# Optimization experiments

Measured on AMD Instinct MI355X. Metric: run time of the kernel, lower is better.

Reference implementation:

```python
import jax, jax.numpy as jnp
import numpy as np

B, SQ, SE, SI, SEI = 16, 512, 512, 256, 768
D, H = 1024, 16
DK = D // H
L1, L2 = 0.5, 0.5
NEG = -1e30  # stand-in for -inf masked_fill


def setup_inputs() -> dict:
    key = jax.random.key(0)
    ks = jax.random.split(key, 32)
    f = lambda i, shp: jax.random.normal(ks[i], shp, dtype=jnp.float32)
    w = lambda i: f(i, (D, D)) * (1.0 / np.sqrt(D))
    b = lambda i: jnp.zeros((D,), jnp.float32)
    inp = {
        'q': f(0, (B, SQ, D)),
        'k_e': f(1, (B, SE, D)), 'v_e': f(2, (B, SE, D)),
        'k_i': f(3, (B, SI, D)), 'v_i': f(4, (B, SI, D)),
        'k_ei': f(5, (B, SEI, D)), 'v_ei': f(6, (B, SEI, D)),
        'mask_e': jax.random.randint(ks[7], (B, SQ, SE), 0, 2) == 1,
        'mask_ei': jax.random.randint(ks[8], (B, SQ, SEI), 0, 2) == 1,
        'e_padding_mask': jax.random.randint(ks[9], (B, SE), 0, 2) == 1,
        'ei_padding_mask': jax.random.randint(ks[10], (B, SEI), 0, 2) == 1,
        'Wq': w(11), 'bq': b(11),
        'Wke': w(12), 'bke': b(12), 'Wve': w(13), 'bve': b(13),
        'Wki': w(14), 'bki': b(14), 'Wvi': w(15), 'bvi': b(15),
        'Wkei': w(16), 'bkei': b(16), 'Wvei': w(17), 'bvei': b(17),
        'Wout': w(18), 'bout': b(18),
    }
    return inp


def _proj(x, W, b):
    # (B, S, D) -> (B, H, S, DK)
    B_, S_, _ = x.shape
    return (x @ W + b).reshape(B_, S_, H, DK).transpose(0, 2, 1, 3)


def _attn(qh, kh, vh, mask, pad_mask):
    # qh: (B,H,Sq,DK), kh/vh: (B,H,Sk,DK)
    s = jnp.einsum('bhqd,bhkd->bhqk', qh, kh) / np.sqrt(DK)
    if mask is not None:
        s = jnp.where(mask[:, None, :, :], NEG, s)
    if pad_mask is not None:
        s = jnp.where(pad_mask[:, None, None, :], NEG, s)
    w = jax.nn.softmax(s, axis=-1)
    # dropout in original is applied to a discarded temp (eval / no-op)
    return jnp.einsum('bhqk,bhkd->bhqd', w, vh), w


def reference(q, k_e, k_i, k_ei, v_e, v_i, v_ei,
              mask_e, mask_ei, e_padding_mask, ei_padding_mask,
              Wq, bq, Wke, bke, Wve, bve, Wki, bki, Wvi, bvi,
              Wkei, bkei, Wvei, bvei, Wout, bout):
    qh = _proj(q, Wq, bq)
    o_e, aw_e = _attn(qh, _proj(k_e, Wke, bke), _proj(v_e, Wve, bve), mask_e, e_padding_mask)
    o_i, aw_i = _attn(qh, _proj(k_i, Wki, bki), _proj(v_i, Wvi, bvi), None, None)
    o_ei, _ = _attn(qh, _proj(k_ei, Wkei, bkei), _proj(v_ei, Wvei, bvei), mask_ei, ei_padding_mask)
    scores = o_e + L1 * o_i + L2 * o_ei  # (B,H,Sq,DK)
    concat = scores.transpose(0, 2, 1, 3).reshape(B, SQ, D)
    output = concat @ Wout + bout
    return output, aw_e, aw_i
```

## Files before the change

kernel.cpp:

```cpp
#include <hip/hip_runtime.h>
#include <stdint.h>

typedef __attribute__((ext_vector_type(8))) short bf16x8;
typedef __attribute__((ext_vector_type(4))) short s16x4;
typedef __attribute__((ext_vector_type(4))) float f32x4;

__device__ __forceinline__ short f2bf(float f){
  unsigned x = __float_as_uint(f);
  unsigned r = (x + 0x7fffu + ((x >> 16) & 1u)) >> 16;
  return (short)r;
}

__device__ __forceinline__ void g2l16(const void* g, void* l){
  __builtin_amdgcn_global_load_lds(
      (const __attribute__((address_space(1))) unsigned int*)(unsigned long long)(uintptr_t)g,
      (__attribute__((address_space(3))) unsigned int*)(unsigned int)(uintptr_t)l,
      16, 0, 0);
}

struct C3 { const float* in[3]; short* out[3]; };
__global__ __launch_bounds__(256) void cvt3(C3 c){
  const float* __restrict__ in = c.in[blockIdx.z];
  short* __restrict__ out = c.out[blockIdx.z];
  const int i = blockIdx.x * 256 + threadIdx.x;
  const float4* p = (const float4*)in + (size_t)i * 2;
  const float4 a = p[0], b = p[1];
  bf16x8 v;
  v[0] = f2bf(a.x); v[1] = f2bf(a.y); v[2] = f2bf(a.z); v[3] = f2bf(a.w);
  v[4] = f2bf(b.x); v[5] = f2bf(b.y); v[6] = f2bf(b.z); v[7] = f2bf(b.w);
  *(bf16x8*)(out + (size_t)i * 8) = v;
}

__global__ __launch_bounds__(256)
void make_bits(const int* __restrict__ mask, const int* __restrict__ pad,
               unsigned* __restrict__ bits, int SK){
  const int s = blockIdx.x * 256 + threadIdx.x;
  const size_t row = blockIdx.y;
  const int b = (int)(row >> 9);
  const bool v = (mask[row * SK + s] != 0) || (pad[(size_t)b * SK + s] != 0);
  unsigned long long bal = __ballot(v);
  const int lane = threadIdx.x & 63;
  if ((lane & 31) == 0)
    bits[(row * SK + s) >> 5] = (unsigned)(bal >> (lane & 32));
}

struct W8 { const float* w[8]; };
__global__ __launch_bounds__(256) void pack_w8(W8 ws8, short* __restrict__ out){
  const int m = blockIdx.y;
  const float* __restrict__ W = ws8.w[m];
  short* o = out + (size_t)m * 1048576 + (size_t)blockIdx.x * 4096;
  const int kt = blockIdx.x & 31, nt = blockIdx.x >> 5;
  const int t = threadIdx.x;
  #pragma unroll
  for (int i = 0; i < 16; ++i){
    int flat = i * 256 + t;
    int kl = flat >> 7;
    int nl = flat & 127;
    o[nl * 32 + kl] = f2bf(W[(size_t)(kt * 32 + kl) * 1024 + nt * 128 + nl]);
  }
}

struct GSeg { const short* A; const short* Wp; const float* bias; void* C; int om; int S; };
struct G3 { GSeg s[3]; };
__global__ __launch_bounds__(256)
void gemm128b(G3 g){
  const GSeg sg = g.s[blockIdx.z];
  __shared__ short sA[2][4096];
  __shared__ short sB[2][4096];
  const int t = threadIdx.x;
  const int m0 = blockIdx.x * 128;
  const int nt = blockIdx.y;
  const int n0 = nt * 128;
  const int w = t >> 6, lane = t & 63, lr = lane & 15, lg = lane >> 4;
  const int wm = (w >> 1) * 64, wn = (w & 1) * 64;

  const int arow  = t >> 2;
  const int acol8 = (t & 3) * 8;
  const short* Ag = sg.A + (size_t)(m0 + arow) * 1024 + acol8;
  const short* Bg = sg.Wp + (size_t)nt * 32 * 4096 + t * 8;

  f32x4 acc[4][4] = {};

  {
    g2l16(Ag, sA[0] + t * 8);
    g2l16(Ag + 64 * 1024, sA[0] + 2048 + t * 8);
    g2l16(Bg, sB[0] + t * 8);
    g2l16(Bg + 2048, sB[0] + 2048 + t * 8);
  }

  int cur = 0;
  for (int kt = 0; kt < 32; ++kt){
    __syncthreads();
    if (kt < 31){
      const int kn = kt + 1;
      g2l16(Ag + kn * 32, sA[cur ^ 1] + t * 8);
      g2l16(Ag + 64 * 1024 + kn * 32, sA[cur ^ 1] + 2048 + t * 8);
      const short* bt = Bg + (size_t)kn * 4096;
      g2l16(bt, sB[cur ^ 1] + t * 8);
      g2l16(bt + 2048, sB[cur ^ 1] + 2048 + t * 8);
    }

    bf16x8 af[4], bfr[4];
    #pragma unroll
    for (int mi = 0; mi < 4; ++mi)
      af[mi] = *(const bf16x8*)&sA[cur][(wm + mi * 16 + lr) * 32 + lg * 8];
    #pragma unroll
    for (int ni = 0; ni < 4; ++ni)
      bfr[ni] = *(const bf16x8*)&sB[cur][(wn + ni * 16 + lr) * 32 + lg * 8];
    #pragma unroll
    for (int mi = 0; mi < 4; ++mi)
      #pragma unroll
      for (int ni = 0; ni < 4; ++ni)
        acc[mi][ni] = __builtin_amdgcn_mfma_f32_16x16x32_bf16(
            af[mi], bfr[ni], acc[mi][ni], 0, 0, 0);
    cur ^= 1;
  }

  #pragma unroll
  for (int ni = 0; ni < 4; ++ni){
    const int n = n0 + wn + ni * 16 + lr;
    const float bv = sg.bias[n];
    #pragma unroll
    for (int mi = 0; mi < 4; ++mi){
      const int mb = m0 + wm + mi * 16 + lg * 4;
      if (sg.om == 0){
        short* C = (short*)sg.C;
        #pragma unroll
        for (int j = 0; j < 4; ++j)
          C[(size_t)(mb + j) * 1024 + n] = f2bf(acc[mi][ni][j] + bv);
      } else if (sg.om == 1){
        short* C = (short*)sg.C;
        const int bb = mb / sg.S, sb = mb % sg.S;
        const int hh = n >> 6, dk = n & 63;
        s16x4 pk;
        #pragma unroll
        for (int j = 0; j < 4; ++j) pk[j] = f2bf(acc[mi][ni][j] + bv);
        *(s16x4*)&((short*)sg.C)[(((size_t)bb * 16 + hh) * 64 + dk) * sg.S + sb] = pk;
      } else {
        float* C = (float*)sg.C;
        #pragma unroll
        for (int j = 0; j < 4; ++j)
          C[(size_t)(mb + j) * 1024 + n] = acc[mi][ni][j] + bv;
      }
    }
  }
}

template<int SK, bool HAS_BIAS, bool SINGLE>
__device__ __forceinline__ void attn_mod(
    const short* __restrict__ Kp, const short* __restrict__ Vt,
    const unsigned* __restrict__ bits, float* __restrict__ aw,
    const bf16x8 (&qf)[2], f32x4 (&tot)[4], float wgt,
    short* sK, short* sV, short* sPw,
    int b, int h, int qw, int w, int lane, int lr, int lg){
  constexpr int NT  = SK / 128;
  constexpr int SKW = SK / 32;

  const int kchunk = (lane & 7) ^ ((lane >> 3) & 7);
  const short* Ksrc = Kp + ((size_t)b * SK + w * 32 + (lane >> 3)) * 1024 + h * 64 + kchunk * 8;
  short* sKd = sK + w * 2048 + lane * 8;
  short* sVd = sV + w * 2048 + lane * 8;
  const short* Vsrc = Vt + ((size_t)(b * 16 + h)) * 64 * SK;

  const unsigned* bitrow[4];
  if (HAS_BIAS){
    #pragma unroll
    for (int j = 0; j < 4; ++j)
      bitrow[j] = bits + ((size_t)(b * 512 + qw + lg * 4 + j)) * SKW;
  }

  float lrow[4];
  #pragma unroll
  for (int j = 0; j < 4; ++j) lrow[j] = 0.f;
  f32x4 acco[4] = {};

  if (!SINGLE){
    for (int tt = 0; tt < NT; ++tt){
      const int s0 = tt * 128;
      __syncthreads();
      #pragma unroll
      for (int i = 0; i < 4; ++i)
        g2l16(Ksrc + ((size_t)s0 + i * 8) * 1024, sKd + i * 512);
      __syncthreads();

      f32x4 accs[8];
      #pragma unroll
      for (int si = 0; si < 8; ++si){
        f32x4 a = {};
        #pragma unroll
        for (int dt = 0; dt < 2; ++dt){
          bf16x8 kf = *(const bf16x8*)&sK[(si * 16 + lr) * 64 + ((dt * 4 + lg) ^ (lr & 7)) * 8];
          a = __builtin_amdgcn_mfma_f32_16x16x32_bf16(qf[dt], kf, a, 0, 0, 0);
        }
        accs[si] = a;
      }

      #pragma unroll
      for (int j = 0; j < 4; ++j){
        unsigned wb[4];
        if (HAS_BIAS){
          #pragma unroll
          for (int sp = 0; sp < 4; ++sp) wb[sp] = bitrow[j][(s0 >> 5) + sp];
        }
        float ssum = 0.f;
        #pragma unroll
        for (int si = 0; si < 8; ++si){
          float v = accs[si][j] * 0.125f;
          if (HAS_BIAS && ((wb[si >> 1] >> ((si & 1) * 16 + lr)) & 1u)) v = -1e30f;
          ssum += __expf(v);
        }
        lrow[j] += ssum;
      }
    }

    #pragma unroll
    for (int j = 0; j < 4; ++j){
      #pragma unroll
      for (int d = 1; d < 16; d <<= 1) lrow[j] += __shfl_xor(lrow[j], d);
    }
    float rinv[4];
    #pragma unroll
    for (int j = 0; j < 4; ++j) rinv[j] = lrow[j] > 0.f ? 1.0f / lrow[j] : 0.f;

    for (int tt = 0; tt < NT; ++tt){
      const int s0 = tt * 128;
      __syncthreads();
      #pragma unroll
      for (int i = 0; i < 4; ++i)
        g2l16(Ksrc + ((size_t)s0 + i * 8) * 1024, sKd + i * 512);
      #pragma unroll
      for (int i = 0; i < 4; ++i){
        const int dd = w * 16 + i * 4 + (lane >> 4);
        const int cg = (lane & 15) ^ ((i * 4 + (lane >> 4)) & 15);
        g2l16(Vsrc + (size_t)dd * SK + s0 + cg * 8, sVd + i * 512);
      }
      __syncthreads();

      f32x4 accs[8];
      #pragma unroll
      for (int si = 0; si < 8; ++si){
        f32x4 a = {};
        #pragma unroll
        for (int dt = 0; dt < 2; ++dt){
          bf16x8 kf = *(const bf16x8*)&sK[(si * 16 + lr) * 64 + ((dt * 4 + lg) ^ (lr & 7)) * 8];
          a = __builtin_amdgcn_mfma_f32_16x16x32_bf16(qf[dt], kf, a, 0, 0, 0);
        }
        accs[si] = a;
      }

      #pragma unroll
      for (int half = 0; half < 2; ++half){
        #pragma unroll
        for (int j = 0; j < 4; ++j){
          unsigned wb[2];
          if (HAS_BIAS){
            #pragma unroll
            for (int sp = 0; sp < 2; ++sp) wb[sp] = bitrow[j][(s0 >> 5) + half * 2 + sp];
          }
          const int qq = lg * 4 + j;
          float* awrow = aw + (((size_t)(b * 16 + h)) * 512 + qw + qq) * SK + s0 + half * 64 + lr;
          #pragma unroll
          for (int si2 = 0; si2 < 4; ++si2){
            const int si = half * 4 + si2;
            float v = accs[si][j] * 0.125f;
            if (HAS_BIAS && ((wb[si2 >> 1] >> ((si2 & 1) * 16 + lr)) & 1u)) v = -1e30f;
            const float p = __expf(v) * rinv[j];
            __builtin_nontemporal_store(p, &awrow[si2 * 16]);
            sPw[qq * 64 + (((si2 * 2 + (lr >> 3)) ^ (qq & 7)) * 8) + (lr & 7)] = f2bf(p);
          }
        }
        #pragma unroll
        for (int kt2 = 0; kt2 < 2; ++kt2){
          const int kt = half * 2 + kt2;
          bf16x8 pa = *(const bf16x8*)&sPw[lr * 64 + (((kt2 * 4 + lg) ^ (lr & 7)) * 8)];
          #pragma unroll
          for (int ni = 0; ni < 4; ++ni){
            bf16x8 vf = *(const bf16x8*)&sV[(ni * 16 + lr) * 128 + ((kt * 4 + lg) ^ lr) * 8];
            acco[ni] = __builtin_amdgcn_mfma_f32_16x16x32_bf16(pa, vf, acco[ni], 0, 0, 0);
          }
        }
      }
    }

    #pragma unroll
    for (int ni = 0; ni < 4; ++ni)
      #pragma unroll
      for (int j = 0; j < 4; ++j)
        tot[ni][j] += wgt * acco[ni][j];
  } else {
    for (int tt = 0; tt < NT; ++tt){
      const int s0 = tt * 128;
      __syncthreads();
      #pragma unroll
      for (int i = 0; i < 4; ++i)
        g2l16(Ksrc + ((size_t)s0 + i * 8) * 1024, sKd + i * 512);
      #pragma unroll
      for (int i = 0; i < 4; ++i){
        const int dd = w * 16 + i * 4 + (lane >> 4);
        const int cg = (lane & 15) ^ ((i * 4 + (lane >> 4)) & 15);
        g2l16(Vsrc + (size_t)dd * SK + s0 + cg * 8, sVd + i * 512);
      }
      __syncthreads();

      f32x4 accs[8];
      #pragma unroll
      for (int si = 0; si < 8; ++si){
        f32x4 a = {};
        #pragma unroll
        for (int dt = 0; dt < 2; ++dt){
          bf16x8 kf = *(const bf16x8*)&sK[(si * 16 + lr) * 64 + ((dt * 4 + lg) ^ (lr & 7)) * 8];
          a = __builtin_amdgcn_mfma_f32_16x16x32_bf16(qf[dt], kf, a, 0, 0, 0);
        }
        accs[si] = a;
      }

      #pragma unroll
      for (int half = 0; half < 2; ++half){
        #pragma unroll
        for (int j = 0; j < 4; ++j){
          unsigned wb[2];
          if (HAS_BIAS){
            #pragma unroll
            for (int sp = 0; sp < 2; ++sp) wb[sp] = bitrow[j][(s0 >> 5) + half * 2 + sp];
          }
          const int qq = lg * 4 + j;
          float ls = 0.f;
          #pragma unroll
          for (int si2 = 0; si2 < 4; ++si2){
            const int si = half * 4 + si2;
            float v = accs[si][j] * 0.125f;
            if (HAS_BIAS && ((wb[si2 >> 1] >> ((si2 & 1) * 16 + lr)) & 1u)) v = -1e30f;
            const float p = __expf(v);
            ls += p;
            sPw[qq * 64 + (((si2 * 2 + (lr >> 3)) ^ (qq & 7)) * 8) + (lr & 7)] = f2bf(p);
          }
          lrow[j] += ls;
        }
        #pragma unroll
        for (int kt2 = 0; kt2 < 2; ++kt2){
          const int kt = half * 2 + kt2;
          bf16x8 pa = *(const bf16x8*)&sPw[lr * 64 + (((kt2 * 4 + lg) ^ (lr & 7)) * 8)];
          #pragma unroll
          for (int ni = 0; ni < 4; ++ni){
            bf16x8 vf = *(const bf16x8*)&sV[(ni * 16 + lr) * 128 + ((kt * 4 + lg) ^ lr) * 8];
            acco[ni] = __builtin_amdgcn_mfma_f32_16x16x32_bf16(pa, vf, acco[ni], 0, 0, 0);
          }
        }
      }
    }

    #pragma unroll
    for (int j = 0; j < 4; ++j){
      #pragma unroll
      for (int d = 1; d < 16; d <<= 1) lrow[j] += __shfl_xor(lrow[j], d);
      const float r = lrow[j] > 0.f ? wgt / lrow[j] : 0.f;
      #pragma unroll
      for (int ni = 0; ni < 4; ++ni) tot[ni][j] += r * acco[ni][j];
    }
  }
}

__global__ __launch_bounds__(256)
void attn_fused(const short* __restrict__ Qp,
                const short* __restrict__ Kep, const short* __restrict__ Vte,
                const unsigned* __restrict__ bits_e, float* __restrict__ aw_e,
                const short* __restrict__ Kip, const short* __restrict__ Vti,
                float* __restrict__ aw_i,
                const short* __restrict__ Keip, const short* __restrict__ Vtei,
                const unsigned* __restrict__ bits_ei,
                short* __restrict__ concat){
  __shared__ short sK[8192];
  __shared__ short sV[8192];
  __shared__ short sP[4096];

  const int bid = blockIdx.x;
  const int qt = bid >> 8;
  const int g  = bid & 255;
  const int h = g & 15, b = g >> 4;
  const int q0 = qt * 64;
  const int t = threadIdx.x, w = t >> 6, lane = t & 63;
  const int lr = lane & 15, lg = lane >> 4;
  const int qw = q0 + w * 16;
  short* sPw = sP + w * 1024;

  const short* Qb = Qp + ((size_t)(b * 512 + qw + lr)) * 1024 + h * 64;
  bf16x8 qf[2];
  qf[0] = *(const bf16x8*)&Qb[lg * 8];
  qf[1] = *(const bf16x8*)&Qb[32 + lg * 8];

  f32x4 tot[4] = {};

  attn_mod<512, true , false>(Kep,  Vte,  bits_e,  aw_e, qf, tot, 1.0f,
                              sK, sV, sPw, b, h, qw, w, lane, lr, lg);
  attn_mod<256, false, false>(Kip,  Vti,  nullptr, aw_i, qf, tot, 0.5f,
                              sK, sV, sPw, b, h, qw, w, lane, lr, lg);
  attn_mod<768, true , true >(Keip, Vtei, bits_ei, nullptr, qf, tot, 0.5f,
                              sK, sV, sPw, b, h, qw, w, lane, lr, lg);

  #pragma unroll
  for (int ni = 0; ni < 4; ++ni)
    #pragma unroll
    for (int j = 0; j < 4; ++j){
      const size_t addr = ((size_t)(b * 512 + qw + lg * 4 + j)) * 1024 + h * 64 + ni * 16 + lr;
      concat[addr] = f2bf(tot[ni][j]);
    }
}

extern "C" void kernel_launch(void* const* d_in, const int* in_sizes, int n_in,
                              void* d_out, int out_size, void* d_ws, size_t ws_size,
                              hipStream_t stream){
  const float* q    = (const float*)d_in[0];
  const float* k_e  = (const float*)d_in[1];
  const float* v_e  = (const float*)d_in[2];
  const float* k_i  = (const float*)d_in[3];
  const float* v_i  = (const float*)d_in[4];
  const float* k_ei = (const float*)d_in[5];
  const float* v_ei = (const float*)d_in[6];
  const int* mask_e  = (const int*)d_in[7];
  const int* mask_ei = (const int*)d_in[8];
  const int* pad_e   = (const int*)d_in[9];
  const int* pad_ei  = (const int*)d_in[10];
  const float* Wq   = (const float*)d_in[11]; const float* bq   = (const float*)d_in[12];
  const float* Wke  = (const float*)d_in[13]; const float* bke  = (const float*)d_in[14];
  const float* Wve  = (const float*)d_in[15]; const float* bve  = (const float*)d_in[16];
  const float* Wki  = (const float*)d_in[17]; const float* bki  = (const float*)d_in[18];
  const float* Wvi  = (const float*)d_in[19]; const float* bvi  = (const float*)d_in[20];
  const float* Wkei = (const float*)d_in[21]; const float* bkei = (const float*)d_in[22];
  const float* Wvei = (const float*)d_in[23]; const float* bvei = (const float*)d_in[24];
  const float* Wout = (const float*)d_in[25]; const float* bout = (const float*)d_in[26];

  char* ws = (char*)d_ws;
  const size_t MB = 1048576;
  short* PW     = (short*)(ws);
  short* St0    = (short*)(ws + 16 * MB);
  short* St1    = (short*)(ws + 32 * MB);
  short* St2    = (short*)(ws + 48 * MB);
  short* St1c   = (short*)(ws + 40 * MB);
  unsigned* bits_e  = (unsigned*)(ws + 64 * MB);
  unsigned* bits_ei = (unsigned*)(ws + 66 * MB);
  short* Qp     = (short*)(ws + 69 * MB);
  short* Kep    = (short*)(ws + 85 * MB);
  short* Kip    = (short*)(ws + 101 * MB);
  short* Keip   = (short*)(ws + 109 * MB);
  short* Vte    = (short*)(ws + 133 * MB);
  short* Vti    = (short*)(ws + 149 * MB);
  short* Vtei   = (short*)(ws + 157 * MB);
  short* concat = (short*)(ws + 181 * MB);

  float* out0 = (float*)d_out;
  float* aw_e = out0 + 8388608;
  float* aw_i = out0 + 75497472;

  W8 w8;
  w8.w[0] = Wq;  w8.w[1] = Wke;  w8.w[2] = Wve;  w8.w[3] = Wki;
  w8.w[4] = Wvi; w8.w[5] = Wkei; w8.w[6] = Wvei; w8.w[7] = Wout;
  pack_w8<<<dim3(256, 8), 256, 0, stream>>>(w8, PW);

  {
    C3 c; c.in[0] = q; c.in[1] = k_e; c.in[2] = v_e;
    c.out[0] = St0; c.out[1] = St1; c.out[2] = St2;
    cvt3<<<dim3(4096, 1, 3), 256, 0, stream>>>(c);
    G3 gg;
    gg.s[0] = {St0, PW + 0 * 1048576, bq,  Qp,  0, 512};
    gg.s[1] = {St1, PW + 1 * 1048576, bke, Kep, 0, 512};
    gg.s[2] = {St2, PW + 2 * 1048576, bve, Vte, 1, 512};
    gemm128b<<<dim3(64, 8, 3), 256, 0, stream>>>(gg);
  }
  {
    C3 c; c.in[0] = k_i; c.in[1] = v_i; c.in[2] = k_i;
    c.out[0] = St0; c.out[1] = St1; c.out[2] = St0;
    cvt3<<<dim3(2048, 1, 2), 256, 0, stream>>>(c);
    G3 gg;
    gg.s[0] = {St0, PW + 3 * 1048576, bki, Kip, 0, 256};
    gg.s[1] = {St1, PW + 4 * 1048576, bvi, Vti, 1, 256};
    gg.s[2] = gg.s[0];
    gemm128b<<<dim3(32, 8, 2), 256, 0, stream>>>(gg);
  }
  {
    C3 c; c.in[0] = k_ei; c.in[1] = v_ei; c.in[2] = k_ei;
    c.out[0] = St0; c.out[1] = St1c; c.out[2] = St0;
    cvt3<<<dim3(6144, 1, 2), 256, 0, stream>>>(c);
    G3 gg;
    gg.s[0] = {St0,  PW + 5 * 1048576, bkei, Keip, 0, 768};
    gg.s[1] = {St1c, PW + 6 * 1048576, bvei, Vtei, 1, 768};
    gg.s[2] = gg.s[0];
    gemm128b<<<dim3(96, 8, 2), 256, 0, stream>>>(gg);
  }

  make_bits<<<dim3(2, 8192), 256, 0, stream>>>(mask_e,  pad_e,  bits_e,  512);
  make_bits<<<dim3(3, 8192), 256, 0, stream>>>(mask_ei, pad_ei, bits_ei, 768);

  attn_fused<<<2048, 256, 0, stream>>>(Qp, Kep, Vte, bits_e, aw_e,
                                       Kip, Vti, aw_i, Keip, Vtei, bits_ei, concat);

  {
    G3 gg;
    gg.s[0] = {concat, PW + 7 * 1048576, bout, out0, 2, 512};
    gg.s[1] = gg.s[0]; gg.s[2] = gg.s[0];
    gemm128b<<<dim3(64, 8, 1), 256, 0, stream>>>(gg);
  }
}
```

Measured before the change: 579.6 us.

## Use 128-query attention blocks with 512 threads and merge K/V projection launches

The fused attention kernel now runs 512 threads per block over 128 query rows. Each wave loads half as much of every shared K/V tile, so each tile staged in LDS serves twice as many queries and global K/V traffic is halved. Separately, the k_i/v_i and k_ei/v_ei conversions and projection GEMMs are merged into one cvt4 and one gemm128b launch, using per-segment bounds and early-exit blocks, and workspace buffers are remapped to fit. The larger blocks raise LDS use and the register pressure per block, which may lower occupancy, and the merged GEMM grid has idle blocks for the shorter segments.

```diff
diff --git a/kernel.cpp b/kernel.cpp
--- a/kernel.cpp
+++ b/kernel.cpp
@@ -18,17 +18,17 @@
       16, 0, 0);
 }
 
-struct C3 { const float* in[3]; short* out[3]; };
-__global__ __launch_bounds__(256) void cvt3(C3 c){
-  const float* __restrict__ in = c.in[blockIdx.z];
-  short* __restrict__ out = c.out[blockIdx.z];
+struct C4 { const float* in[4]; short* out[4]; int n8[4]; };
+__global__ __launch_bounds__(256) void cvt4(C4 c){
+  const int z = blockIdx.z;
   const int i = blockIdx.x * 256 + threadIdx.x;
-  const float4* p = (const float4*)in + (size_t)i * 2;
+  if (i >= c.n8[z]) return;
+  const float4* p = (const float4*)c.in[z] + (size_t)i * 2;
   const float4 a = p[0], b = p[1];
   bf16x8 v;
   v[0] = f2bf(a.x); v[1] = f2bf(a.y); v[2] = f2bf(a.z); v[3] = f2bf(a.w);
   v[4] = f2bf(b.x); v[5] = f2bf(b.y); v[6] = f2bf(b.z); v[7] = f2bf(b.w);
-  *(bf16x8*)(out + (size_t)i * 8) = v;
+  *(bf16x8*)(c.out[z] + (size_t)i * 8) = v;
 }
 
 __global__ __launch_bounds__(256)
@@ -60,11 +60,12 @@
   }
 }
 
-struct GSeg { const short* A; const short* Wp; const float* bias; void* C; int om; int S; };
-struct G3 { GSeg s[3]; };
+struct GSeg { const short* A; const short* Wp; const float* bias; void* C; int om; int S; int mt; };
+struct G4 { GSeg s[4]; };
 __global__ __launch_bounds__(256)
-void gemm128b(G3 g){
+void gemm128b(G4 g){
   const GSeg sg = g.s[blockIdx.z];
+  if (blockIdx.x >= sg.mt) return;
   __shared__ short sA[2][4096];
   __shared__ short sB[2][4096];
   const int t = threadIdx.x;
@@ -135,7 +136,7 @@
         s16x4 pk;
         #pragma unroll
         for (int j = 0; j < 4; ++j) pk[j] = f2bf(acc[mi][ni][j] + bv);
-        *(s16x4*)&((short*)sg.C)[(((size_t)bb * 16 + hh) * 64 + dk) * sg.S + sb] = pk;
+        *(s16x4*)&C[(((size_t)bb * 16 + hh) * 64 + dk) * sg.S + sb] = pk;
       } else {
         float* C = (float*)sg.C;
         #pragma unroll
@@ -157,9 +158,9 @@
   constexpr int SKW = SK / 32;
 
   const int kchunk = (lane & 7) ^ ((lane >> 3) & 7);
-  const short* Ksrc = Kp + ((size_t)b * SK + w * 32 + (lane >> 3)) * 1024 + h * 64 + kchunk * 8;
-  short* sKd = sK + w * 2048 + lane * 8;
-  short* sVd = sV + w * 2048 + lane * 8;
+  const short* Ksrc = Kp + ((size_t)b * SK + w * 16 + (lane >> 3)) * 1024 + h * 64 + kchunk * 8;
+  short* sKd = sK + w * 1024 + lane * 8;
+  short* sVd = sV + w * 1024 + lane * 8;
   const short* Vsrc = Vt + ((size_t)(b * 16 + h)) * 64 * SK;
 
   const unsigned* bitrow[4];
@@ -178,9 +179,8 @@
     for (int tt = 0; tt < NT; ++tt){
       const int s0 = tt * 128;
       __syncthreads();
-      #pragma unroll
-      for (int i = 0; i < 4; ++i)
-        g2l16(Ksrc + ((size_t)s0 + i * 8) * 1024, sKd + i * 512);
+      g2l16(Ksrc + (size_t)s0 * 1024, sKd);
+      g2l16(Ksrc + (size_t)(s0 + 8) * 1024, sKd + 512);
       __syncthreads();
 
       f32x4 accs[8];
@@ -225,13 +225,12 @@
     for (int tt = 0; tt < NT; ++tt){
       const int s0 = tt * 128;
       __syncthreads();
-      #pragma unroll
-      for (int i = 0; i < 4; ++i)
-        g2l16(Ksrc + ((size_t)s0 + i * 8) * 1024, sKd + i * 512);
-      #pragma unroll
-      for (int i = 0; i < 4; ++i){
-        const int dd = w * 16 + i * 4 + (lane >> 4);
-        const int cg = (lane & 15) ^ ((i * 4 + (lane >> 4)) & 15);
+      g2l16(Ksrc + (size_t)s0 * 1024, sKd);
+      g2l16(Ksrc + (size_t)(s0 + 8) * 1024, sKd + 512);
+      #pragma unroll
+      for (int i = 0; i < 2; ++i){
+        const int dd = w * 8 + i * 4 + (lane >> 4);
+        const int cg = (lane & 15) ^ (dd & 15);
         g2l16(Vsrc + (size_t)dd * SK + s0 + cg * 8, sVd + i * 512);
       }
       __syncthreads();
@@ -291,13 +290,12 @@
     for (int tt = 0; tt < NT; ++tt){
       const int s0 = tt * 128;
       __syncthreads();
-      #pragma unroll
-      for (int i = 0; i < 4; ++i)
-        g2l16(Ksrc + ((size_t)s0 + i * 8) * 1024, sKd + i * 512);
-      #pragma unroll
-      for (int i = 0; i < 4; ++i){
-        const int dd = w * 16 + i * 4 + (lane >> 4);
-        const int cg = (lane & 15) ^ ((i * 4 + (lane >> 4)) & 15);
+      g2l16(Ksrc + (size_t)s0 * 1024, sKd);
+      g2l16(Ksrc + (size_t)(s0 + 8) * 1024, sKd + 512);
+      #pragma unroll
+      for (int i = 0; i < 2; ++i){
+        const int dd = w * 8 + i * 4 + (lane >> 4);
+        const int cg = (lane & 15) ^ (dd & 15);
         g2l16(Vsrc + (size_t)dd * SK + s0 + cg * 8, sVd + i * 512);
       }
       __syncthreads();
@@ -360,7 +358,7 @@
   }
 }
 
-__global__ __launch_bounds__(256)
+__global__ __launch_bounds__(512)
 void attn_fused(const short* __restrict__ Qp,
                 const short* __restrict__ Kep, const short* __restrict__ Vte,
                 const unsigned* __restrict__ bits_e, float* __restrict__ aw_e,
@@ -371,13 +369,13 @@
                 short* __restrict__ concat){
   __shared__ short sK[8192];
   __shared__ short sV[8192];
-  __shared__ short sP[4096];
+  __shared__ short sP[8192];
 
   const int bid = blockIdx.x;
   const int qt = bid >> 8;
   const int g  = bid & 255;
   const int h = g & 15, b = g >> 4;
-  const int q0 = qt * 64;
+  const int q0 = qt * 128;
   const int t = threadIdx.x, w = t >> 6, lane = t & 63;
   const int lr = lane & 15, lg = lane >> 4;
   const int qw = q0 + w * 16;
@@ -432,20 +430,23 @@
   char* ws = (char*)d_ws;
   const size_t MB = 1048576;
   short* PW     = (short*)(ws);
-  short* St0    = (short*)(ws + 16 * MB);
-  short* St1    = (short*)(ws + 32 * MB);
-  short* St2    = (short*)(ws + 48 * MB);
-  short* St1c   = (short*)(ws + 40 * MB);
-  unsigned* bits_e  = (unsigned*)(ws + 64 * MB);
-  unsigned* bits_ei = (unsigned*)(ws + 66 * MB);
-  short* Qp     = (short*)(ws + 69 * MB);
-  short* Kep    = (short*)(ws + 85 * MB);
-  short* Kip    = (short*)(ws + 101 * MB);
-  short* Keip   = (short*)(ws + 109 * MB);
-  short* Vte    = (short*)(ws + 133 * MB);
-  short* Vti    = (short*)(ws + 149 * MB);
-  short* Vtei   = (short*)(ws + 157 * MB);
-  short* concat = (short*)(ws + 181 * MB);
+  short* StA0   = (short*)(ws + 16 * MB);
+  short* StA1   = (short*)(ws + 32 * MB);
+  short* StA2   = (short*)(ws + 48 * MB);
+  short* StB0   = (short*)(ws + 16 * MB);
+  short* StB1   = (short*)(ws + 24 * MB);
+  short* StC0   = (short*)(ws + 32 * MB);
+  short* StC1   = (short*)(ws + 56 * MB);
+  unsigned* bits_e  = (unsigned*)(ws + 80 * MB);
+  unsigned* bits_ei = (unsigned*)(ws + 82 * MB);
+  short* Qp     = (short*)(ws + 85 * MB);
+  short* Kep    = (short*)(ws + 101 * MB);
+  short* Kip    = (short*)(ws + 117 * MB);
+  short* Keip   = (short*)(ws + 125 * MB);
+  short* Vte    = (short*)(ws + 149 * MB);
+  short* Vti    = (short*)(ws + 165 * MB);
+  short* Vtei   = (short*)(ws + 173 * MB);
+  short* concat = (short*)(ws + 16 * MB);
 
   float* out0 = (float*)d_out;
   float* aw_e = out0 + 8388608;
@@ -457,46 +458,44 @@
   pack_w8<<<dim3(256, 8), 256, 0, stream>>>(w8, PW);
 
   {
-    C3 c; c.in[0] = q; c.in[1] = k_e; c.in[2] = v_e;
-    c.out[0] = St0; c.out[1] = St1; c.out[2] = St2;
-    cvt3<<<dim3(4096, 1, 3), 256, 0, stream>>>(c);
-    G3 gg;
-    gg.s[0] = {St0, PW + 0 * 1048576, bq,  Qp,  0, 512};
-    gg.s[1] = {St1, PW + 1 * 1048576, bke, Kep, 0, 512};
-    gg.s[2] = {St2, PW + 2 * 1048576, bve, Vte, 1, 512};
+    C4 c;
+    c.in[0] = q;   c.out[0] = StA0; c.n8[0] = 1048576;
+    c.in[1] = k_e; c.out[1] = StA1; c.n8[1] = 1048576;
+    c.in[2] = v_e; c.out[2] = StA2; c.n8[2] = 1048576;
+    c.in[3] = q;   c.out[3] = StA0; c.n8[3] = 0;
+    cvt4<<<dim3(4096, 1, 3), 256, 0, stream>>>(c);
+    G4 gg;
+    gg.s[0] = {StA0, PW + 0 * 1048576, bq,  Qp,  0, 512, 64};
+    gg.s[1] = {StA1, PW + 1 * 1048576, bke, Kep, 0, 512, 64};
+    gg.s[2] = {StA2, PW + 2 * 1048576, bve, Vte, 1, 512, 64};
+    gg.s[3] = gg.s[0];
     gemm128b<<<dim3(64, 8, 3), 256, 0, stream>>>(gg);
   }
   {
-    C3 c; c.in[0] = k_i; c.in[1] = v_i; c.in[2] = k_i;
-    c.out[0] = St0; c.out[1] = St1; c.out[2] = St0;
-    cvt3<<<dim3(2048, 1, 2), 256, 0, stream>>>(c);
-    G3 gg;
-    gg.s[0] = {St0, PW + 3 * 1048576, bki, Kip, 0, 256};
-    gg.s[1] = {St1, PW + 4 * 1048576, bvi, Vti, 1, 256};
-    gg.s[2] = gg.s[0];
-    gemm128b<<<dim3(32, 8, 2), 256, 0, stream>>>(gg);
-  }
-  {
-    C3 c; c.in[0] = k_ei; c.in[1] = v_ei; c.in[2] = k_ei;
-    c.out[0] = St0; c.out[1] = St1c; c.out[2] = St0;
-    cvt3<<<dim3(6144, 1, 2), 256, 0, stream>>>(c);
-    G3 gg;
-    gg.s[0] = {St0,  PW + 5 * 1048576, bkei, Keip, 0, 768};
-    gg.s[1] = {St1c, PW + 6 * 1048576, bvei, Vtei, 1, 768};
-    gg.s[2] = gg.s[0];
-    gemm128b<<<dim3(96, 8, 2), 256, 0, stream>>>(gg);
+    C4 c;
+    c.in[0] = k_i;  c.out[0] = StB0; c.n8[0] = 524288;
+    c.in[1] = v_i;  c.out[1] = StB1; c.n8[1] = 524288;
+    c.in[2] = k_ei; c.out[2] = StC0; c.n8[2] = 1572864;
+    c.in[3] = v_ei; c.out[3] = StC1; c.n8[3] = 1572864;
+    cvt4<<<dim3(6144, 1, 4), 256, 0, stream>>>(c);
+    G4 gg;
+    gg.s[0] = {StB0, PW + 3 * 1048576, bki,  Kip,  0, 256, 32};
+    gg.s[1] = {StB1, PW + 4 * 1048576, bvi,  Vti,  1, 256, 32};
+    gg.s[2] = {StC0, PW + 5 * 1048576, bkei, Keip, 0, 768, 96};
+    gg.s[3] = {StC1, PW + 6 * 1048576, bvei, Vtei, 1, 768, 96};
+    gemm128b<<<dim3(96, 8, 4), 256, 0, stream>>>(gg);
   }
 
   make_bits<<<dim3(2, 8192), 256, 0, stream>>>(mask_e,  pad_e,  bits_e,  512);
   make_bits<<<dim3(3, 8192), 256, 0, stream>>>(mask_ei, pad_ei, bits_ei, 768);
 
-  attn_fused<<<2048, 256, 0, stream>>>(Qp, Kep, Vte, bits_e, aw_e,
+  attn_fused<<<1024, 512, 0, stream>>>(Qp, Kep, Vte, bits_e, aw_e,
                                        Kip, Vti, aw_i, Keip, Vtei, bits_ei, concat);
 
   {
-    G3 gg;
-    gg.s[0] = {concat, PW + 7 * 1048576, bout, out0, 2, 512};
-    gg.s[1] = gg.s[0]; gg.s[2] = gg.s[0];
+    G4 gg;
+    gg.s[0] = {concat, PW + 7 * 1048576, bout, out0, 2, 512, 64};
+    gg.s[1] = gg.s[0]; gg.s[2] = gg.s[0]; gg.s[3] = gg.s[0];
     gemm128b<<<dim3(64, 8, 1), 256, 0, stream>>>(gg);
   }
 }
```

New measurement: 542.0 us. -6.5%, faster.
